# Optimization experiments

Hardware: AMD Instinct MI355X
Metric: run time of the kernel (lower is better)

The kernel has to match this reference:

```python
import jax, jax.numpy as jnp
import numpy as np

EMBED = 128
HEADS = 8
HDIM = EMBED // HEADS  # 16
LN_EPS = 1e-5


def _angle_decay():
    # angle: 1/10000**linspace(0,1,HDIM//2), each value repeated twice -> (HDIM,)
    a = 1.0 / 10000 ** jnp.linspace(0.0, 1.0, HDIM // 2)
    angle = jnp.repeat(a, 2)
    # decay: log(1 - 2^(-initial_value - heads_range*h/H)), initial_value=1, heads_range=3
    h = jnp.arange(HEADS, dtype=jnp.float32)
    decay = jnp.log1p(-jnp.exp2(-(1.0 + 3.0 * h / HEADS)))
    return angle, decay


def _rotary(t, sin, cos):
    # t: (..., S, D); sin/cos: (S, D)
    return t * cos + jnp.concatenate([-t[..., 1::2], t[..., ::2]], axis=-1) * sin


def _layer_norm(x, g, b):
    mu = jnp.mean(x, axis=-1, keepdims=True)
    var = jnp.mean((x - mu) ** 2, axis=-1, keepdims=True)
    return (x - mu) * jax.lax.rsqrt(var + LN_EPS) * g + b


def setup_inputs() -> dict:
    key = jax.random.key(0)
    ks = jax.random.split(key, 6)
    B, N, C = 32, 8192, EMBED
    s = 0.02
    return {
        "x": jax.random.normal(ks[0], (B, N, C), dtype=jnp.float32),
        "wq": jax.random.normal(ks[1], (C, C), dtype=jnp.float32) * s,
        "bq": jnp.zeros((C,), jnp.float32),
        "wk": jax.random.normal(ks[2], (C, C), dtype=jnp.float32) * s,
        "bk": jnp.zeros((C,), jnp.float32),
        "wv": jax.random.normal(ks[3], (C, C), dtype=jnp.float32) * s,
        "bv": jnp.zeros((C,), jnp.float32),
        "ln1_g": jnp.ones((C,), jnp.float32),
        "ln1_b": jnp.zeros((C,), jnp.float32),
        "ffn_w1": jax.random.normal(ks[4], (C, 4 * C), dtype=jnp.float32) * s,
        "ffn_b1": jnp.zeros((4 * C,), jnp.float32),
        "ffn_w2": jax.random.normal(ks[5], (4 * C, C), dtype=jnp.float32) * s,
        "ffn_b2": jnp.zeros((C,), jnp.float32),
        "ln2_g": jnp.ones((C,), jnp.float32),
        "ln2_b": jnp.zeros((C,), jnp.float32),
    }


def reference(x, wq, bq, wk, bk, wv, bv, ln1_g, ln1_b,
              ffn_w1, ffn_b1, ffn_w2, ffn_b2, ln2_g, ln2_b):
    B, N, C = x.shape  # attention runs over B (frames), per location N
    xt = jnp.transpose(x, (1, 0, 2))  # (N, B, C)
    S = B  # seq_len for pos encoder

    angle, decay = _angle_decay()
    idx = jnp.arange(S, dtype=jnp.float32)
    sin = jnp.sin(idx[:, None] * angle[None, :])  # (S, HDIM)
    cos = jnp.cos(idx[:, None] * angle[None, :])
    # decay mask: |i - j| * decay_h -> (H, S, S)
    dist = jnp.abs(idx[:, None] - idx[None, :])
    mask = dist[None, :, :] * decay[:, None, None]

    def proj(w, b):
        t = xt @ w + b  # (N, S, C)
        return jnp.transpose(t.reshape(N, S, HEADS, HDIM), (2, 0, 1, 3))  # (H, N, S, D)

    q = _rotary(proj(wq, bq), sin, cos)
    k = _rotary(proj(wk, bk), sin, cos)
    v = proj(wv, bv)

    scores = jnp.einsum('hnqd,hnkd->hnqk', q, k) + mask[:, None, :, :]
    attn = jax.nn.softmax(scores, axis=-1)  # dropout is identity in eval
    out = jnp.einsum('hnqk,hnkd->hnqd', attn, v)  # (H, N, S, D)
    out = jnp.transpose(out, (1, 2, 0, 3)).reshape(N, S, C)

    out = _layer_norm(out + xt, ln1_g, ln1_b)
    ffn = jax.nn.relu(out @ ffn_w1 + ffn_b1) @ ffn_w2 + ffn_b2
    out = _layer_norm(ffn + out, ln2_g, ln2_b)
    return jnp.transpose(out, (1, 0, 2))  # (B, N, C)
```

## Files before the change

### kernel.cpp

```cpp
#include <hip/hip_runtime.h>
#include <hip/hip_bf16.h>


#define NN 8192
#define BS 32
#define CC 128
#define HH 8
#define DD 16
#define FF 512
#define QS 129

typedef __attribute__((ext_vector_type(8))) short bf16x8;
typedef __attribute__((ext_vector_type(4))) float f32x4;
typedef __attribute__((ext_vector_type(4))) unsigned int u32x4;
typedef __attribute__((ext_vector_type(2))) unsigned int u32x2;

#define XB_H 0
#define QB_H 4352
#define KB_H 8704
#define VT_H 13056
#define TAB_F 8832
#define P_H 4352
#define P_HEAD 1152
#define P_STR 36
#define O_H 13568
#define O1B_H 0
#define H_H 4096
#define LDS_BYTES 40960

__device__ inline unsigned short f2bf(float f) {
  return __builtin_bit_cast(unsigned short, __float2bfloat16(f));
}
__device__ inline unsigned pk2bf(float lo, float hi) {
  return (unsigned)f2bf(lo) | ((unsigned)f2bf(hi) << 16);
}
__device__ inline float bf2f(unsigned short h) {
  unsigned u = ((unsigned)h) << 16;
  return __builtin_bit_cast(float, u);
}

__global__ void pack_weights(const float* __restrict__ wq, const float* __restrict__ wk,
                             const float* __restrict__ wv, const float* __restrict__ w1,
                             const float* __restrict__ w2, unsigned short* __restrict__ outp)
{
  const int id = blockIdx.x * 256 + threadIdx.x;
  if (id >= 23040) return;
  if (id >= 22528) {
    const int i = id - 22528;
    const int s = i >> 4, d = i & 15;
    const float a = exp2f(-1.89824462565f * (float)(d >> 1));
    const float ang = (float)s * a;
    float2* tab = (float2*)(outp + 180224);
    tab[i] = make_float2(sinf(ang), cosf(ang));
    return;
  }
  const int l = id & 63;
  const int chunk = id >> 6;
  const float* W; int ldw, colbase, k0;
  if (chunk < 96) {
    const int ct = chunk >> 2, kk = chunk & 3;
    W = (ct < 8) ? wq : (ct < 16) ? wk : wv;
    ldw = CC; colbase = (ct & 7) * 16 + (l & 15); k0 = kk * 32 + (l >> 4) * 8;
  } else if (chunk < 224) {
    const int c2 = chunk - 96, ct = c2 >> 2, kk = c2 & 3;
    W = w1; ldw = FF; colbase = ct * 16 + (l & 15); k0 = kk * 32 + (l >> 4) * 8;
  } else {
    const int c2 = chunk - 224, ct = c2 >> 4, kk = c2 & 15;
    W = w2; ldw = CC; colbase = ct * 16 + (l & 15); k0 = kk * 32 + (l >> 4) * 8;
  }
  unsigned int o[4];
  #pragma unroll
  for (int jj = 0; jj < 4; ++jj)
    o[jj] = pk2bf(W[(size_t)(k0 + 2 * jj) * ldw + colbase],
                  W[(size_t)(k0 + 2 * jj + 1) * ldw + colbase]);
  *(u32x4*)(outp + (size_t)id * 8) = (u32x4){o[0], o[1], o[2], o[3]};
}

__global__ __launch_bounds__(512, 6) void fused_mfma(
    const float* __restrict__ x,
    const float* __restrict__ bq, const float* __restrict__ bk, const float* __restrict__ bv,
    const float* __restrict__ ln1g, const float* __restrict__ ln1b,
    const float* __restrict__ b1, const float* __restrict__ b2,
    const float* __restrict__ ln2g, const float* __restrict__ ln2b,
    const unsigned short* __restrict__ wpack,
    const float2* __restrict__ rott,
    float* __restrict__ out)
{
  extern __shared__ char smem[];
  float* ldsf = (float*)smem;
  unsigned short* ldsh = (unsigned short*)smem;
  const int n = blockIdx.x;
  const int t = threadIdx.x;
  const int w = t >> 6;
  const int l = t & 63;
  const int lr = l & 15;
  const int lg = l >> 4;

  {
    const int s = t >> 4, c0 = (t & 15) * 8;
    const float* xp = x + ((size_t)s * NN + n) * CC + c0;
    const float4 v0 = *(const float4*)xp;
    const float4 v1 = *(const float4*)(xp + 4);
    u32x4 pk;
    pk[0] = pk2bf(v0.x, v0.y);
    pk[1] = pk2bf(v0.z, v0.w);
    pk[2] = pk2bf(v1.x, v1.y);
    pk[3] = pk2bf(v1.z, v1.w);
    *(u32x4*)(ldsh + XB_H + s * 136 + c0) = pk;
    ((float2*)(ldsf + TAB_F))[t] = rott[t];
  }
  __syncthreads();

  {
    f32x4 acc[2][3];
    #pragma unroll
    for (int c = 0; c < 3; ++c) {
      const int ct = 3 * w + c;
      const int col = (ct & 7) * 16 + lr;
      const float* bb = (ct < 8) ? bq : (ct < 16) ? bk : bv;
      const float b = bb[col];
      acc[0][c] = (f32x4){b, b, b, b};
      acc[1][c] = acc[0][c];
    }
    #pragma unroll
    for (int kk = 0; kk < 4; ++kk) {
      const bf16x8 a0 = *(const bf16x8*)(ldsh + XB_H + lr * 136 + kk * 32 + lg * 8);
      const bf16x8 a1 = *(const bf16x8*)(ldsh + XB_H + (16 + lr) * 136 + kk * 32 + lg * 8);
      #pragma unroll
      for (int c = 0; c < 3; ++c) {
        const int ct = 3 * w + c;
        const bf16x8 b = *(const bf16x8*)(wpack + ((size_t)(ct * 4 + kk) * 64 + l) * 8);
        acc[0][c] = __builtin_amdgcn_mfma_f32_16x16x32_bf16(a0, b, acc[0][c], 0, 0, 0);
        acc[1][c] = __builtin_amdgcn_mfma_f32_16x16x32_bf16(a1, b, acc[1][c], 0, 0, 0);
      }
    }
    float sn[2][4], cs[2][4];
    if (3 * w < 16) {
      #pragma unroll
      for (int rt = 0; rt < 2; ++rt)
        #pragma unroll
        for (int e = 0; e < 4; ++e) {
          const int row = rt * 16 + lg * 4 + e;
          const float2 tc = ((const float2*)(ldsf + TAB_F))[row * 16 + lr];
          sn[rt][e] = tc.x;
          cs[rt][e] = tc.y;
        }
    }
    const int pd = (lr < 8) ? (2 * lr + 1) : (2 * lr - 16);
    const float sgn = (lr < 8) ? -1.0f : 1.0f;
    const int psrc = (l & 48) | pd;
    #pragma unroll
    for (int c = 0; c < 3; ++c) {
      const int ct = 3 * w + c;
      if (ct < 16) {
        const int dst = (ct < 8) ? QB_H : KB_H;
        const int colbase = (ct & 7) * 16;
        #pragma unroll
        for (int rt = 0; rt < 2; ++rt)
          #pragma unroll
          for (int e = 0; e < 4; ++e) {
            const float v = acc[rt][c][e];
            const float pv = __shfl(v, psrc);
            const float r = v * cs[rt][e] + sgn * pv * sn[rt][e];
            ldsh[dst + (rt * 16 + lg * 4 + e) * 136 + colbase + lr] = f2bf(r);
          }
      } else {
        const int hv = ct - 16;
        #pragma unroll
        for (int rt = 0; rt < 2; ++rt)
          #pragma unroll
          for (int e = 0; e < 4; ++e)
            ldsh[VT_H + hv * 576 + lr * 36 + rt * 16 + lg * 4 + e] = f2bf(acc[rt][c][e]);
      }
    }
  }
  __syncthreads();

  {
    const int h16 = w * 16;
    const float dec = log1pf(-exp2f(-(1.0f + 0.375f * (float)w)));
    const bf16x8 z = {};
    bf16x8 Ak[2], Bq[2];
    #pragma unroll
    for (int kt = 0; kt < 2; ++kt)
      Ak[kt] = (lg < 2) ? *(const bf16x8*)(ldsh + KB_H + (kt * 16 + lr) * 136 + h16 + lg * 8) : z;
    #pragma unroll
    for (int qt = 0; qt < 2; ++qt)
      Bq[qt] = (lg < 2) ? *(const bf16x8*)(ldsh + QB_H + (qt * 16 + lr) * 136 + h16 + lg * 8) : z;
    const bf16x8 Bv = *(const bf16x8*)(ldsh + VT_H + w * 576 + lr * 36 + lg * 8);
    __syncthreads();

    f32x4 accs[2][2];
    #pragma unroll
    for (int kt = 0; kt < 2; ++kt)
      #pragma unroll
      for (int qt = 0; qt < 2; ++qt) {
        #pragma unroll
        for (int e = 0; e < 4; ++e) {
          const int q = qt * 16 + lr;
          const int k = kt * 16 + lg * 4 + e;
          accs[kt][qt][e] = fabsf((float)(q - k)) * dec;
        }
        accs[kt][qt] = __builtin_amdgcn_mfma_f32_16x16x32_bf16(Ak[kt], Bq[qt], accs[kt][qt], 0, 0, 0);
      }
    unsigned short* Pl = ldsh + P_H + w * P_HEAD;
    #pragma unroll
    for (int qt = 0; qt < 2; ++qt) {
      float mx = accs[0][qt][0];
      #pragma unroll
      for (int kt = 0; kt < 2; ++kt)
        #pragma unroll
        for (int e = 0; e < 4; ++e) mx = fmaxf(mx, accs[kt][qt][e]);
      mx = fmaxf(mx, __shfl_xor(mx, 16));
      mx = fmaxf(mx, __shfl_xor(mx, 32));
      float p[2][4];
      float sm = 0.0f;
      #pragma unroll
      for (int kt = 0; kt < 2; ++kt)
        #pragma unroll
        for (int e = 0; e < 4; ++e) { p[kt][e] = __expf(accs[kt][qt][e] - mx); sm += p[kt][e]; }
      sm += __shfl_xor(sm, 16);
      sm += __shfl_xor(sm, 32);
      const float inv = 1.0f / sm;
      #pragma unroll
      for (int kt = 0; kt < 2; ++kt) {
        u32x2 pw;
        pw[0] = pk2bf(p[kt][0] * inv, p[kt][1] * inv);
        pw[1] = pk2bf(p[kt][2] * inv, p[kt][3] * inv);
        *(u32x2*)(Pl + (qt * 16 + lr) * P_STR + kt * 16 + lg * 4) = pw;
      }
    }
    #pragma unroll
    for (int qt = 0; qt < 2; ++qt) {
      const bf16x8 Ap = *(const bf16x8*)(Pl + (qt * 16 + lr) * P_STR + lg * 8);
      f32x4 z4 = {0.0f, 0.0f, 0.0f, 0.0f};
      const f32x4 o = __builtin_amdgcn_mfma_f32_16x16x32_bf16(Ap, Bv, z4, 0, 0, 0);
      #pragma unroll
      for (int e = 0; e < 4; ++e)
        ldsh[O_H + (qt * 16 + lg * 4 + e) * 136 + h16 + lr] = f2bf(o[e]);
    }
  }
  __syncthreads();

  {
    const int row = t >> 4, sub = t & 15;
    const unsigned short* Or = ldsh + O_H + row * 136 + sub * 8;
    const unsigned short* Xr = ldsh + XB_H + row * 136 + sub * 8;
    float v[8];
    #pragma unroll
    for (int i = 0; i < 8; ++i) v[i] = bf2f(Or[i]) + bf2f(Xr[i]);
    float sum = 0.0f;
    #pragma unroll
    for (int i = 0; i < 8; ++i) sum += v[i];
    #pragma unroll
    for (int m = 1; m < 16; m <<= 1) sum += __shfl_xor(sum, m);
    const float mu = sum * (1.0f / 128.0f);
    float s2 = 0.0f;
    #pragma unroll
    for (int i = 0; i < 8; ++i) { const float d = v[i] - mu; s2 += d * d; }
    #pragma unroll
    for (int m = 1; m < 16; m <<= 1) s2 += __shfl_xor(s2, m);
    const float rstd = rsqrtf(s2 * (1.0f / 128.0f) + 1e-5f);
    u32x4 pk;
    #pragma unroll
    for (int i = 0; i < 4; ++i) {
      const int c = sub * 8 + 2 * i;
      pk[i] = pk2bf((v[2 * i] - mu) * rstd * ln1g[c] + ln1b[c],
                    (v[2 * i + 1] - mu) * rstd * ln1g[c + 1] + ln1b[c + 1]);
    }
    __syncthreads();
    *(u32x4*)(ldsh + O1B_H + row * 128 + ((sub * 8) ^ ((row & 7) << 3))) = pk;
  }
  __syncthreads();

  {
    f32x4 acc1[2][4];
    #pragma unroll
    for (int c = 0; c < 4; ++c) {
      const float b = b1[(4 * w + c) * 16 + lr];
      acc1[0][c] = (f32x4){b, b, b, b};
      acc1[1][c] = acc1[0][c];
    }
    #pragma unroll
    for (int kk = 0; kk < 4; ++kk) {
      const int csw = (kk * 32 + lg * 8) ^ ((lr & 7) << 3);
      const bf16x8 a0 = *(const bf16x8*)(ldsh + O1B_H + lr * 128 + csw);
      const bf16x8 a1 = *(const bf16x8*)(ldsh + O1B_H + (16 + lr) * 128 + csw);
      #pragma unroll
      for (int c = 0; c < 4; ++c) {
        const int chunk = 96 + (4 * w + c) * 4 + kk;
        const bf16x8 b = *(const bf16x8*)(wpack + ((size_t)chunk * 64 + l) * 8);
        acc1[0][c] = __builtin_amdgcn_mfma_f32_16x16x32_bf16(a0, b, acc1[0][c], 0, 0, 0);
        acc1[1][c] = __builtin_amdgcn_mfma_f32_16x16x32_bf16(a1, b, acc1[1][c], 0, 0, 0);
      }
    }
    #pragma unroll
    for (int p = 0; p < 2; ++p)
      #pragma unroll
      for (int c = 0; c < 4; ++c) {
        const int col = (4 * w + c) * 16 + lr;
        #pragma unroll
        for (int e = 0; e < 4; ++e) {
          const int row = p * 16 + lg * 4 + e;
          ldsh[H_H + row * 512 + (col ^ ((row & 7) << 3))] = f2bf(fmaxf(acc1[p][c][e], 0.0f));
        }
      }
  }
  __syncthreads();

  {
    const int col = w * 16 + lr;
    const float b = b2[col];
    f32x4 acc2[2];
    acc2[0] = (f32x4){b, b, b, b};
    acc2[1] = acc2[0];
    #pragma unroll
    for (int kk = 0; kk < 16; ++kk) {
      const int csw = (kk * 32 + lg * 8) ^ ((lr & 7) << 3);
      const bf16x8 a0 = *(const bf16x8*)(ldsh + H_H + lr * 512 + csw);
      const bf16x8 a1 = *(const bf16x8*)(ldsh + H_H + (16 + lr) * 512 + csw);
      const int chunk = 224 + w * 16 + kk;
      const bf16x8 bb = *(const bf16x8*)(wpack + ((size_t)chunk * 64 + l) * 8);
      acc2[0] = __builtin_amdgcn_mfma_f32_16x16x32_bf16(a0, bb, acc2[0], 0, 0, 0);
      acc2[1] = __builtin_amdgcn_mfma_f32_16x16x32_bf16(a1, bb, acc2[1], 0, 0, 0);
    }
    #pragma unroll
    for (int p = 0; p < 2; ++p)
      #pragma unroll
      for (int e = 0; e < 4; ++e) {
        const int srow = p * 16 + lg * 4 + e;
        const int idx = O1B_H + srow * 128 + (col ^ ((srow & 7) << 3));
        const float res = bf2f(ldsh[idx]);
        ldsh[idx] = f2bf(acc2[p][e] + res);
      }
  }
  __syncthreads();

  {
    const int row = t >> 4, sub = t & 15;
    const unsigned short* Or = ldsh + O1B_H + row * 128 + ((sub * 8) ^ ((row & 7) << 3));
    float v[8];
    #pragma unroll
    for (int i = 0; i < 8; ++i) v[i] = bf2f(Or[i]);
    float sum = 0.0f;
    #pragma unroll
    for (int i = 0; i < 8; ++i) sum += v[i];
    #pragma unroll
    for (int m = 1; m < 16; m <<= 1) sum += __shfl_xor(sum, m);
    const float mu = sum * (1.0f / 128.0f);
    float s2 = 0.0f;
    #pragma unroll
    for (int i = 0; i < 8; ++i) { const float d = v[i] - mu; s2 += d * d; }
    #pragma unroll
    for (int m = 1; m < 16; m <<= 1) s2 += __shfl_xor(s2, m);
    const float rstd = rsqrtf(s2 * (1.0f / 128.0f) + 1e-5f);
    const int c0 = sub * 8;
    float4 r0, r1;
    r0.x = (v[0] - mu) * rstd * ln2g[c0 + 0] + ln2b[c0 + 0];
    r0.y = (v[1] - mu) * rstd * ln2g[c0 + 1] + ln2b[c0 + 1];
    r0.z = (v[2] - mu) * rstd * ln2g[c0 + 2] + ln2b[c0 + 2];
    r0.w = (v[3] - mu) * rstd * ln2g[c0 + 3] + ln2b[c0 + 3];
    r1.x = (v[4] - mu) * rstd * ln2g[c0 + 4] + ln2b[c0 + 4];
    r1.y = (v[5] - mu) * rstd * ln2g[c0 + 5] + ln2b[c0 + 5];
    r1.z = (v[6] - mu) * rstd * ln2g[c0 + 6] + ln2b[c0 + 6];
    r1.w = (v[7] - mu) * rstd * ln2g[c0 + 7] + ln2b[c0 + 7];
    float* op = out + ((size_t)row * NN + n) * CC + c0;
    *(float4*)op = r0;
    *(float4*)(op + 4) = r1;
  }
}

__global__ __launch_bounds__(512, 4) void fused_retention_block(
    const float* __restrict__ x,
    const float* __restrict__ wq, const float* __restrict__ bq,
    const float* __restrict__ wk, const float* __restrict__ bk,
    const float* __restrict__ wv, const float* __restrict__ bv,
    const float* __restrict__ ln1g, const float* __restrict__ ln1b,
    const float* __restrict__ w1, const float* __restrict__ b1,
    const float* __restrict__ w2, const float* __restrict__ b2,
    const float* __restrict__ ln2g, const float* __restrict__ ln2b,
    float* __restrict__ out)
{
  const int n = blockIdx.x;
  const int t = threadIdx.x;
  __shared__ float SM[3 * BS * QS];
  float* Qs = SM;
  float* Ks = SM + BS * QS;
  float* Vs = SM + 2 * BS * QS;
  {
    const int o4 = t & 31;
    const int sp = t >> 5;
    const float* xr0 = x + ((size_t)(2 * sp) * NN + n) * CC;
    const float* xr1 = xr0 + (size_t)NN * CC;
    for (int m = 0; m < 3; ++m) {
      const float* W  = (m == 0) ? wq : (m == 1) ? wk : wv;
      const float* bb = (m == 0) ? bq : (m == 1) ? bk : bv;
      float* O = SM + m * BS * QS;
      float b4[4];
      *(float4*)b4 = *(const float4*)(bb + o4 * 4);
      float a0[4] = {b4[0], b4[1], b4[2], b4[3]};
      float a1[4] = {b4[0], b4[1], b4[2], b4[3]};
      for (int c4 = 0; c4 < 32; ++c4) {
        float xa4[4], xb4[4];
        *(float4*)xa4 = *(const float4*)(xr0 + c4 * 4);
        *(float4*)xb4 = *(const float4*)(xr1 + c4 * 4);
        const float* wp = W + (c4 * 4) * CC + o4 * 4;
        #pragma unroll
        for (int j = 0; j < 4; ++j) {
          float w4[4];
          *(float4*)w4 = *(const float4*)(wp + j * CC);
          #pragma unroll
          for (int e = 0; e < 4; ++e) { a0[e] += xa4[j] * w4[e]; a1[e] += xb4[j] * w4[e]; }
        }
      }
      float* q0 = O + (2 * sp) * QS + o4 * 4;
      float* q1 = O + (2 * sp + 1) * QS + o4 * 4;
      #pragma unroll
      for (int e = 0; e < 4; ++e) { q0[e] = a0[e]; q1[e] = a1[e]; }
    }
  }
  __syncthreads();
  {
    const int tt = t & 255;
    const int s = tt >> 3;
    const int h = tt & 7;
    float* row = ((t < 256) ? Qs : Ks) + s * QS + h * DD;
    float v[DD];
    #pragma unroll
    for (int d = 0; d < DD; ++d) v[d] = row[d];
    #pragma unroll
    for (int d = 0; d < DD; ++d) {
      const int j = d >> 1;
      const float a = exp2f(-1.89824462565f * (float)j);
      const float ang = (float)s * a;
      const float sn = sinf(ang);
      const float cs = cosf(ang);
      const float rot = (d < 8) ? -v[2 * d + 1] : v[2 * (d - 8)];
      row[d] = v[d] * cs + rot * sn;
    }
  }
  __syncthreads();
  if (t < 256) {
    const int h = t >> 5;
    const int qi = t & 31;
    const float dec = log1pf(-exp2f(-(1.0f + 0.375f * (float)h)));
    float q[DD];
    const float* Qr = Qs + qi * QS + h * DD;
    #pragma unroll
    for (int d = 0; d < DD; ++d) q[d] = Qr[d];
    float sc[BS];
    float mx = -3.0e38f;
    #pragma unroll
    for (int jj = 0; jj < BS; ++jj) {
      const float* Kr = Ks + jj * QS + h * DD;
      float acc = fabsf((float)(qi - jj)) * dec;
      #pragma unroll
      for (int d = 0; d < DD; ++d) acc += q[d] * Kr[d];
      sc[jj] = acc;
      mx = fmaxf(mx, acc);
    }
    float sum = 0.0f;
    #pragma unroll
    for (int jj = 0; jj < BS; ++jj) { const float p = __expf(sc[jj] - mx); sc[jj] = p; sum += p; }
    const float inv = 1.0f / sum;
    float o[DD];
    #pragma unroll
    for (int d = 0; d < DD; ++d) o[d] = 0.0f;
    #pragma unroll
    for (int jj = 0; jj < BS; ++jj) {
      const float p = sc[jj] * inv;
      const float* Vr = Vs + jj * QS + h * DD;
      #pragma unroll
      for (int d = 0; d < DD; ++d) o[d] += p * Vr[d];
    }
    float* Od = Qs + qi * QS + h * DD;
    #pragma unroll
    for (int d = 0; d < DD; ++d) Od[d] = o[d];
  }
  __syncthreads();
  {
    const int row = t >> 4;
    const int sub = t & 15;
    float* Orow = Qs + row * QS + sub * 8;
    const float* xrow = x + ((size_t)row * NN + n) * CC + sub * 8;
    float v[8];
    #pragma unroll
    for (int i = 0; i < 8; ++i) v[i] = Orow[i] + xrow[i];
    float sum = 0.0f;
    #pragma unroll
    for (int i = 0; i < 8; ++i) sum += v[i];
    #pragma unroll
    for (int m = 1; m < 16; m <<= 1) sum += __shfl_xor(sum, m);
    const float mu = sum * (1.0f / 128.0f);
    float s2 = 0.0f;
    #pragma unroll
    for (int i = 0; i < 8; ++i) { const float d = v[i] - mu; s2 += d * d; }
    #pragma unroll
    for (int m = 1; m < 16; m <<= 1) s2 += __shfl_xor(s2, m);
    const float rstd = rsqrtf(s2 * (1.0f / 128.0f) + 1e-5f);
    #pragma unroll
    for (int i = 0; i < 8; ++i) {
      const int c = sub * 8 + i;
      Orow[i] = (v[i] - mu) * rstd * ln1g[c] + ln1b[c];
    }
  }
  __syncthreads();
  float* Hb = Ks;
  const int f4  = t & 127;
  const int sb4 = (t >> 7) * 4;
  const int o4f = t & 31;
  const int sF  = t >> 5;
  for (int p = 0; p < 2; ++p) {
    {
      float acc[4][4];
      float b14[4];
      *(float4*)b14 = *(const float4*)(b1 + f4 * 4);
      #pragma unroll
      for (int i = 0; i < 4; ++i)
        #pragma unroll
        for (int e = 0; e < 4; ++e) acc[i][e] = b14[e];
      const float* O1b = Qs + (p * 16 + sb4) * QS;
      for (int c = 0; c < CC; ++c) {
        float w4[4];
        *(float4*)w4 = *(const float4*)(w1 + c * FF + f4 * 4);
        #pragma unroll
        for (int i = 0; i < 4; ++i) {
          const float xv = O1b[i * QS + c];
          #pragma unroll
          for (int e = 0; e < 4; ++e) acc[i][e] += xv * w4[e];
        }
      }
      #pragma unroll
      for (int i = 0; i < 4; ++i) {
        float4 r;
        r.x = fmaxf(acc[i][0], 0.0f); r.y = fmaxf(acc[i][1], 0.0f);
        r.z = fmaxf(acc[i][2], 0.0f); r.w = fmaxf(acc[i][3], 0.0f);
        *(float4*)(Hb + (sb4 + i) * FF + f4 * 4) = r;
      }
    }
    __syncthreads();
    {
      const int s = p * 16 + sF;
      float acc[4];
      *(float4*)acc = *(const float4*)(b2 + o4f * 4);
      const float* hrow = Hb + sF * FF;
      for (int k = 0; k < FF; ++k) {
        const float hv = hrow[k];
        float w4[4];
        *(float4*)w4 = *(const float4*)(w2 + k * CC + o4f * 4);
        #pragma unroll
        for (int e = 0; e < 4; ++e) acc[e] += hv * w4[e];
      }
      const float* res = Qs + s * QS + o4f * 4;
      #pragma unroll
      for (int e = 0; e < 4; ++e) acc[e] += res[e];
      float sum = acc[0] + acc[1] + acc[2] + acc[3];
      #pragma unroll
      for (int m = 1; m < 32; m <<= 1) sum += __shfl_xor(sum, m);
      const float mu = sum * (1.0f / 128.0f);
      float s2 = 0.0f;
      #pragma unroll
      for (int e = 0; e < 4; ++e) { const float d = acc[e] - mu; s2 += d * d; }
      #pragma unroll
      for (int m = 1; m < 32; m <<= 1) s2 += __shfl_xor(s2, m);
      const float rstd = rsqrtf(s2 * (1.0f / 128.0f) + 1e-5f);
      float4 r;
      const int c0 = o4f * 4;
      r.x = (acc[0] - mu) * rstd * ln2g[c0 + 0] + ln2b[c0 + 0];
      r.y = (acc[1] - mu) * rstd * ln2g[c0 + 1] + ln2b[c0 + 1];
      r.z = (acc[2] - mu) * rstd * ln2g[c0 + 2] + ln2b[c0 + 2];
      r.w = (acc[3] - mu) * rstd * ln2g[c0 + 3] + ln2b[c0 + 3];
      *(float4*)(out + ((size_t)s * NN + n) * CC + c0) = r;
    }
    __syncthreads();
  }
}

extern "C" void kernel_launch(void* const* d_in, const int* in_sizes, int n_in,
                              void* d_out, int out_size, void* d_ws, size_t ws_size,
                              hipStream_t stream) {
  (void)in_sizes; (void)n_in; (void)out_size;
  const float* x    = (const float*)d_in[0];
  const float* wq   = (const float*)d_in[1];
  const float* bq_  = (const float*)d_in[2];
  const float* wk   = (const float*)d_in[3];
  const float* bk_  = (const float*)d_in[4];
  const float* wv   = (const float*)d_in[5];
  const float* bv_  = (const float*)d_in[6];
  const float* ln1g = (const float*)d_in[7];
  const float* ln1b = (const float*)d_in[8];
  const float* w1   = (const float*)d_in[9];
  const float* b1   = (const float*)d_in[10];
  const float* w2   = (const float*)d_in[11];
  const float* b2   = (const float*)d_in[12];
  const float* ln2g = (const float*)d_in[13];
  const float* ln2b = (const float*)d_in[14];
  float* outp = (float*)d_out;

  if (ws_size >= (size_t)364544) {
    unsigned short* wpack = (unsigned short*)d_ws;
    const float2* rott = (const float2*)((const char*)d_ws + 360448);
    pack_weights<<<90, 256, 0, stream>>>(wq, wk, wv, w1, w2, wpack);
    fused_mfma<<<NN, 512, LDS_BYTES, stream>>>(
        x, bq_, bk_, bv_, ln1g, ln1b, b1, b2, ln2g, ln2b, wpack, rott, outp);
  } else {
    fused_retention_block<<<NN, 512, 0, stream>>>(
        x, wq, bq_, wk, bk_, wv, bv_, ln1g, ln1b,
        w1, b1, w2, b2, ln2g, ln2b, outp);
  }
}
```

Measured before the change: 225.9 us.

## Split FFN into two 16-row halves to shrink LDS and raise occupancy

The FFN and second LayerNorm now run in two passes over 16-row halves instead of all 32 rows at once. The hidden-activation LDS buffer and accumulator register arrays halve in size, and launch bounds rise from 6 to 8 blocks per SM. This trades lower LDS and register pressure for higher occupancy, at the cost of extra barriers and re-reading the FFN weights once per half. The LN2 epilogue is remapped to 32 threads per row over 16 rows.

Result: slower. 437.5 us (+93.7%).

```diff
diff --git a/kernel.cpp b/kernel.cpp
--- a/kernel.cpp
+++ b/kernel.cpp
@@ -26,7 +26,7 @@
 #define O_H 13568
 #define O1B_H 0
 #define H_H 4096
-#define LDS_BYTES 40960
+#define LDS_BYTES 39424
 
 __device__ inline unsigned short f2bf(float f) {
   return __builtin_bit_cast(unsigned short, __float2bfloat16(f));
@@ -76,7 +76,7 @@
   *(u32x4*)(outp + (size_t)id * 8) = (u32x4){o[0], o[1], o[2], o[3]};
 }
 
-__global__ __launch_bounds__(512, 6) void fused_mfma(
+__global__ __launch_bounds__(512, 8) void fused_mfma(
     const float* __restrict__ x,
     const float* __restrict__ bq, const float* __restrict__ bk, const float* __restrict__ bv,
     const float* __restrict__ ln1g, const float* __restrict__ ln1b,
@@ -273,100 +273,84 @@
   }
   __syncthreads();
 
-  {
-    f32x4 acc1[2][4];
-    #pragma unroll
-    for (int c = 0; c < 4; ++c) {
-      const float b = b1[(4 * w + c) * 16 + lr];
-      acc1[0][c] = (f32x4){b, b, b, b};
-      acc1[1][c] = acc1[0][c];
-    }
-    #pragma unroll
-    for (int kk = 0; kk < 4; ++kk) {
-      const int csw = (kk * 32 + lg * 8) ^ ((lr & 7) << 3);
-      const bf16x8 a0 = *(const bf16x8*)(ldsh + O1B_H + lr * 128 + csw);
-      const bf16x8 a1 = *(const bf16x8*)(ldsh + O1B_H + (16 + lr) * 128 + csw);
+  for (int p = 0; p < 2; ++p) {
+    {
+      f32x4 acc1[4];
       #pragma unroll
       for (int c = 0; c < 4; ++c) {
-        const int chunk = 96 + (4 * w + c) * 4 + kk;
-        const bf16x8 b = *(const bf16x8*)(wpack + ((size_t)chunk * 64 + l) * 8);
-        acc1[0][c] = __builtin_amdgcn_mfma_f32_16x16x32_bf16(a0, b, acc1[0][c], 0, 0, 0);
-        acc1[1][c] = __builtin_amdgcn_mfma_f32_16x16x32_bf16(a1, b, acc1[1][c], 0, 0, 0);
-      }
-    }
-    #pragma unroll
-    for (int p = 0; p < 2; ++p)
+        const float b = b1[(4 * w + c) * 16 + lr];
+        acc1[c] = (f32x4){b, b, b, b};
+      }
+      #pragma unroll
+      for (int kk = 0; kk < 4; ++kk) {
+        const int csw = (kk * 32 + lg * 8) ^ ((lr & 7) << 3);
+        const bf16x8 a = *(const bf16x8*)(ldsh + O1B_H + (p * 16 + lr) * 128 + csw);
+        #pragma unroll
+        for (int c = 0; c < 4; ++c) {
+          const int chunk = 96 + (4 * w + c) * 4 + kk;
+          const bf16x8 b = *(const bf16x8*)(wpack + ((size_t)chunk * 64 + l) * 8);
+          acc1[c] = __builtin_amdgcn_mfma_f32_16x16x32_bf16(a, b, acc1[c], 0, 0, 0);
+        }
+      }
       #pragma unroll
       for (int c = 0; c < 4; ++c) {
         const int col = (4 * w + c) * 16 + lr;
         #pragma unroll
         for (int e = 0; e < 4; ++e) {
-          const int row = p * 16 + lg * 4 + e;
-          ldsh[H_H + row * 512 + (col ^ ((row & 7) << 3))] = f2bf(fmaxf(acc1[p][c][e], 0.0f));
+          const int r16 = lg * 4 + e;
+          ldsh[H_H + r16 * 512 + (col ^ ((r16 & 7) << 3))] = f2bf(fmaxf(acc1[c][e], 0.0f));
         }
       }
-  }
-  __syncthreads();
-
-  {
-    const int col = w * 16 + lr;
-    const float b = b2[col];
-    f32x4 acc2[2];
-    acc2[0] = (f32x4){b, b, b, b};
-    acc2[1] = acc2[0];
-    #pragma unroll
-    for (int kk = 0; kk < 16; ++kk) {
-      const int csw = (kk * 32 + lg * 8) ^ ((lr & 7) << 3);
-      const bf16x8 a0 = *(const bf16x8*)(ldsh + H_H + lr * 512 + csw);
-      const bf16x8 a1 = *(const bf16x8*)(ldsh + H_H + (16 + lr) * 512 + csw);
-      const int chunk = 224 + w * 16 + kk;
-      const bf16x8 bb = *(const bf16x8*)(wpack + ((size_t)chunk * 64 + l) * 8);
-      acc2[0] = __builtin_amdgcn_mfma_f32_16x16x32_bf16(a0, bb, acc2[0], 0, 0, 0);
-      acc2[1] = __builtin_amdgcn_mfma_f32_16x16x32_bf16(a1, bb, acc2[1], 0, 0, 0);
-    }
-    #pragma unroll
-    for (int p = 0; p < 2; ++p)
+    }
+    __syncthreads();
+
+    {
+      const int col = w * 16 + lr;
+      const float b = b2[col];
+      f32x4 acc2 = {b, b, b, b};
+      #pragma unroll
+      for (int kk = 0; kk < 16; ++kk) {
+        const int csw = (kk * 32 + lg * 8) ^ ((lr & 7) << 3);
+        const bf16x8 a = *(const bf16x8*)(ldsh + H_H + lr * 512 + csw);
+        const int chunk = 224 + w * 16 + kk;
+        const bf16x8 bb = *(const bf16x8*)(wpack + ((size_t)chunk * 64 + l) * 8);
+        acc2 = __builtin_amdgcn_mfma_f32_16x16x32_bf16(a, bb, acc2, 0, 0, 0);
+      }
       #pragma unroll
       for (int e = 0; e < 4; ++e) {
         const int srow = p * 16 + lg * 4 + e;
         const int idx = O1B_H + srow * 128 + (col ^ ((srow & 7) << 3));
         const float res = bf2f(ldsh[idx]);
-        ldsh[idx] = f2bf(acc2[p][e] + res);
-      }
-  }
-  __syncthreads();
-
-  {
-    const int row = t >> 4, sub = t & 15;
-    const unsigned short* Or = ldsh + O1B_H + row * 128 + ((sub * 8) ^ ((row & 7) << 3));
-    float v[8];
-    #pragma unroll
-    for (int i = 0; i < 8; ++i) v[i] = bf2f(Or[i]);
-    float sum = 0.0f;
-    #pragma unroll
-    for (int i = 0; i < 8; ++i) sum += v[i];
-    #pragma unroll
-    for (int m = 1; m < 16; m <<= 1) sum += __shfl_xor(sum, m);
-    const float mu = sum * (1.0f / 128.0f);
-    float s2 = 0.0f;
-    #pragma unroll
-    for (int i = 0; i < 8; ++i) { const float d = v[i] - mu; s2 += d * d; }
-    #pragma unroll
-    for (int m = 1; m < 16; m <<= 1) s2 += __shfl_xor(s2, m);
-    const float rstd = rsqrtf(s2 * (1.0f / 128.0f) + 1e-5f);
-    const int c0 = sub * 8;
-    float4 r0, r1;
-    r0.x = (v[0] - mu) * rstd * ln2g[c0 + 0] + ln2b[c0 + 0];
-    r0.y = (v[1] - mu) * rstd * ln2g[c0 + 1] + ln2b[c0 + 1];
-    r0.z = (v[2] - mu) * rstd * ln2g[c0 + 2] + ln2b[c0 + 2];
-    r0.w = (v[3] - mu) * rstd * ln2g[c0 + 3] + ln2b[c0 + 3];
-    r1.x = (v[4] - mu) * rstd * ln2g[c0 + 4] + ln2b[c0 + 4];
-    r1.y = (v[5] - mu) * rstd * ln2g[c0 + 5] + ln2b[c0 + 5];
-    r1.z = (v[6] - mu) * rstd * ln2g[c0 + 6] + ln2b[c0 + 6];
-    r1.w = (v[7] - mu) * rstd * ln2g[c0 + 7] + ln2b[c0 + 7];
-    float* op = out + ((size_t)row * NN + n) * CC + c0;
-    *(float4*)op = r0;
-    *(float4*)(op + 4) = r1;
+        ldsh[idx] = f2bf(acc2[e] + res);
+      }
+    }
+    __syncthreads();
+
+    {
+      const int r16 = t >> 5, sub5 = t & 31;
+      const int srow = p * 16 + r16;
+      const unsigned short* Or = ldsh + O1B_H + srow * 128 + ((sub5 * 4) ^ ((srow & 7) << 3));
+      float v[4];
+      #pragma unroll
+      for (int i = 0; i < 4; ++i) v[i] = bf2f(Or[i]);
+      float sum = v[0] + v[1] + v[2] + v[3];
+      #pragma unroll
+      for (int m = 1; m < 32; m <<= 1) sum += __shfl_xor(sum, m);
+      const float mu = sum * (1.0f / 128.0f);
+      float s2 = 0.0f;
+      #pragma unroll
+      for (int i = 0; i < 4; ++i) { const float d = v[i] - mu; s2 += d * d; }
+      #pragma unroll
+      for (int m = 1; m < 32; m <<= 1) s2 += __shfl_xor(s2, m);
+      const float rstd = rsqrtf(s2 * (1.0f / 128.0f) + 1e-5f);
+      const int c0 = sub5 * 4;
+      float4 r;
+      r.x = (v[0] - mu) * rstd * ln2g[c0 + 0] + ln2b[c0 + 0];
+      r.y = (v[1] - mu) * rstd * ln2g[c0 + 1] + ln2b[c0 + 1];
+      r.z = (v[2] - mu) * rstd * ln2g[c0 + 2] + ln2b[c0 + 2];
+      r.w = (v[3] - mu) * rstd * ln2g[c0 + 3] + ln2b[c0 + 3];
+      *(float4*)(out + ((size_t)srow * NN + n) * CC + c0) = r;
+    }
   }
 }
 
```

## Run second FFN GEMM in fp8 and reshuffle LDS layout to drop a barrier

Applied to the files above, without the earlier changes.

Packs the second FFN weight matrix to fp8 and stores the ReLU hidden activations as fp8 in LDS, so the second FFN matmul uses fp8 MFMA with half the LDS and weight bytes. The LN1 output now goes in place over the attention output buffer, padded rather than swizzled, which removes one __syncthreads and shrinks the LDS footprint. Precision drops for the hidden activations and W2 (e4m3), and the padded strides may cause different bank conflicts.

New measurement: 199.1 us, median of 2. 1.13x faster.

```diff
diff --git a/kernel.cpp b/kernel.cpp
--- a/kernel.cpp
+++ b/kernel.cpp
@@ -23,10 +23,10 @@
 #define P_H 4352
 #define P_HEAD 1152
 #define P_STR 36
-#define O_H 13568
-#define O1B_H 0
-#define H_H 4096
-#define LDS_BYTES 40960
+#define OO_H 13568
+#define H_STR 520
+#define W2FP8_OFF 229376
+#define LDS_BYTES 39424
 
 __device__ inline unsigned short f2bf(float f) {
   return __builtin_bit_cast(unsigned short, __float2bfloat16(f));
@@ -37,6 +37,41 @@
 __device__ inline float bf2f(unsigned short h) {
   unsigned u = ((unsigned)h) << 16;
   return __builtin_bit_cast(float, u);
+}
+
+__device__ inline unsigned char f2fp8_sw(float x) {
+  unsigned u = __builtin_bit_cast(unsigned, x);
+  unsigned sign = (u >> 31) << 7;
+  float ax = fabsf(x);
+  if (!(ax >= 0.015625f)) {
+    int q = (int)(ax * 512.0f + 0.5f);
+    if (q > 7) return (unsigned char)(sign | 8);
+    return (unsigned char)(sign | q);
+  }
+  if (ax > 448.0f) ax = 448.0f;
+  unsigned au = __builtin_bit_cast(unsigned, ax);
+  int exp = (int)((au >> 23) & 0xff) - 127;
+  unsigned m3 = ((au & 0x7fffff) + 0x80000) >> 20;
+  if (m3 >= 8) { m3 = 0; exp += 1; }
+  if (exp > 8) return (unsigned char)(sign | 0x7e);
+  return (unsigned char)(sign | ((unsigned)(exp + 7) << 3) | m3);
+}
+__device__ inline unsigned char f2fp8(float x) {
+#if defined(__has_builtin) && __has_builtin(__builtin_amdgcn_cvt_pk_fp8_f32)
+  return (unsigned char)(__builtin_amdgcn_cvt_pk_fp8_f32(x, x, 0, false) & 0xff);
+#else
+  return f2fp8_sw(x);
+#endif
+}
+__device__ inline unsigned pack4fp8(float a, float b, float c, float d) {
+#if defined(__has_builtin) && __has_builtin(__builtin_amdgcn_cvt_pk_fp8_f32)
+  int r = __builtin_amdgcn_cvt_pk_fp8_f32(a, b, 0, false);
+  r = __builtin_amdgcn_cvt_pk_fp8_f32(c, d, r, true);
+  return (unsigned)r;
+#else
+  return (unsigned)f2fp8_sw(a) | ((unsigned)f2fp8_sw(b) << 8) |
+         ((unsigned)f2fp8_sw(c) << 16) | ((unsigned)f2fp8_sw(d) << 24);
+#endif
 }
 
 __global__ void pack_weights(const float* __restrict__ wq, const float* __restrict__ wk,
@@ -56,17 +91,27 @@
   }
   const int l = id & 63;
   const int chunk = id >> 6;
+  if (chunk >= 224) {
+    const int c2 = chunk - 224, ct = c2 >> 4, kk = c2 & 15;
+    const int colbase = ct * 16 + (l & 15);
+    const int k0 = kk * 32 + (l >> 4) * 8;
+    float v[8];
+    #pragma unroll
+    for (int jj = 0; jj < 8; ++jj) v[jj] = w2[(size_t)(k0 + jj) * CC + colbase];
+    u32x2 pw;
+    pw[0] = pack4fp8(v[0], v[1], v[2], v[3]);
+    pw[1] = pack4fp8(v[4], v[5], v[6], v[7]);
+    *(u32x2*)((char*)outp + W2FP8_OFF + ((size_t)c2 * 64 + l) * 8) = pw;
+    return;
+  }
   const float* W; int ldw, colbase, k0;
   if (chunk < 96) {
     const int ct = chunk >> 2, kk = chunk & 3;
     W = (ct < 8) ? wq : (ct < 16) ? wk : wv;
     ldw = CC; colbase = (ct & 7) * 16 + (l & 15); k0 = kk * 32 + (l >> 4) * 8;
-  } else if (chunk < 224) {
+  } else {
     const int c2 = chunk - 96, ct = c2 >> 2, kk = c2 & 3;
     W = w1; ldw = FF; colbase = ct * 16 + (l & 15); k0 = kk * 32 + (l >> 4) * 8;
-  } else {
-    const int c2 = chunk - 224, ct = c2 >> 4, kk = c2 & 15;
-    W = w2; ldw = CC; colbase = ct * 16 + (l & 15); k0 = kk * 32 + (l >> 4) * 8;
   }
   unsigned int o[4];
   #pragma unroll
@@ -237,14 +282,14 @@
       const f32x4 o = __builtin_amdgcn_mfma_f32_16x16x32_bf16(Ap, Bv, z4, 0, 0, 0);
       #pragma unroll
       for (int e = 0; e < 4; ++e)
-        ldsh[O_H + (qt * 16 + lg * 4 + e) * 136 + h16 + lr] = f2bf(o[e]);
+        ldsh[OO_H + (qt * 16 + lg * 4 + e) * 136 + h16 + lr] = f2bf(o[e]);
     }
   }
   __syncthreads();
 
   {
     const int row = t >> 4, sub = t & 15;
-    const unsigned short* Or = ldsh + O_H + row * 136 + sub * 8;
+    const unsigned short* Or = ldsh + OO_H + row * 136 + sub * 8;
     const unsigned short* Xr = ldsh + XB_H + row * 136 + sub * 8;
     float v[8];
     #pragma unroll
@@ -268,8 +313,7 @@
       pk[i] = pk2bf((v[2 * i] - mu) * rstd * ln1g[c] + ln1b[c],
                     (v[2 * i + 1] - mu) * rstd * ln1g[c + 1] + ln1b[c + 1]);
     }
-    __syncthreads();
-    *(u32x4*)(ldsh + O1B_H + row * 128 + ((sub * 8) ^ ((row & 7) << 3))) = pk;
+    *(u32x4*)(ldsh + OO_H + row * 136 + sub * 8) = pk;
   }
   __syncthreads();
 
@@ -283,9 +327,8 @@
     }
     #pragma unroll
     for (int kk = 0; kk < 4; ++kk) {
-      const int csw = (kk * 32 + lg * 8) ^ ((lr & 7) << 3);
-      const bf16x8 a0 = *(const bf16x8*)(ldsh + O1B_H + lr * 128 + csw);
-      const bf16x8 a1 = *(const bf16x8*)(ldsh + O1B_H + (16 + lr) * 128 + csw);
+      const bf16x8 a0 = *(const bf16x8*)(ldsh + OO_H + lr * 136 + kk * 32 + lg * 8);
+      const bf16x8 a1 = *(const bf16x8*)(ldsh + OO_H + (16 + lr) * 136 + kk * 32 + lg * 8);
       #pragma unroll
       for (int c = 0; c < 4; ++c) {
         const int chunk = 96 + (4 * w + c) * 4 + kk;
@@ -294,6 +337,7 @@
         acc1[1][c] = __builtin_amdgcn_mfma_f32_16x16x32_bf16(a1, b, acc1[1][c], 0, 0, 0);
       }
     }
+    char* Hb = smem;
     #pragma unroll
     for (int p = 0; p < 2; ++p)
       #pragma unroll
@@ -302,7 +346,7 @@
         #pragma unroll
         for (int e = 0; e < 4; ++e) {
           const int row = p * 16 + lg * 4 + e;
-          ldsh[H_H + row * 512 + (col ^ ((row & 7) << 3))] = f2bf(fmaxf(acc1[p][c][e], 0.0f));
+          Hb[row * H_STR + col] = (char)f2fp8(fmaxf(acc1[p][c][e], 0.0f));
         }
       }
   }
@@ -314,22 +358,22 @@
     f32x4 acc2[2];
     acc2[0] = (f32x4){b, b, b, b};
     acc2[1] = acc2[0];
+    const char* Hb = smem;
+    const char* W2 = (const char*)wpack + W2FP8_OFF;
     #pragma unroll
     for (int kk = 0; kk < 16; ++kk) {
-      const int csw = (kk * 32 + lg * 8) ^ ((lr & 7) << 3);
-      const bf16x8 a0 = *(const bf16x8*)(ldsh + H_H + lr * 512 + csw);
-      const bf16x8 a1 = *(const bf16x8*)(ldsh + H_H + (16 + lr) * 512 + csw);
-      const int chunk = 224 + w * 16 + kk;
-      const bf16x8 bb = *(const bf16x8*)(wpack + ((size_t)chunk * 64 + l) * 8);
-      acc2[0] = __builtin_amdgcn_mfma_f32_16x16x32_bf16(a0, bb, acc2[0], 0, 0, 0);
-      acc2[1] = __builtin_amdgcn_mfma_f32_16x16x32_bf16(a1, bb, acc2[1], 0, 0, 0);
+      const long a0 = *(const long*)(Hb + lr * H_STR + kk * 32 + lg * 8);
+      const long a1 = *(const long*)(Hb + (16 + lr) * H_STR + kk * 32 + lg * 8);
+      const long bb = *(const long*)(W2 + ((size_t)(w * 16 + kk) * 64 + l) * 8);
+      acc2[0] = __builtin_amdgcn_mfma_f32_16x16x32_fp8_fp8(a0, bb, acc2[0], 0, 0, 0);
+      acc2[1] = __builtin_amdgcn_mfma_f32_16x16x32_fp8_fp8(a1, bb, acc2[1], 0, 0, 0);
     }
     #pragma unroll
     for (int p = 0; p < 2; ++p)
       #pragma unroll
       for (int e = 0; e < 4; ++e) {
         const int srow = p * 16 + lg * 4 + e;
-        const int idx = O1B_H + srow * 128 + (col ^ ((srow & 7) << 3));
+        const int idx = OO_H + srow * 136 + col;
         const float res = bf2f(ldsh[idx]);
         ldsh[idx] = f2bf(acc2[p][e] + res);
       }
@@ -338,7 +382,7 @@
 
   {
     const int row = t >> 4, sub = t & 15;
-    const unsigned short* Or = ldsh + O1B_H + row * 128 + ((sub * 8) ^ ((row & 7) << 3));
+    const unsigned short* Or = ldsh + OO_H + row * 136 + sub * 8;
     float v[8];
     #pragma unroll
     for (int i = 0; i < 8; ++i) v[i] = bf2f(Or[i]);
```
